# Performance work log

Hardware: AMD Instinct MI355X
Metric: run time of the kernel (lower is better)

The kernel has to match this reference:

```python
import jax, jax.numpy as jnp
import numpy as np

NUM_EXPERTS = 8
HIDDEN = 2048
EXPERT_DIM = 4096
R = 64
LORA_ALPHA = 16
SCALING = LORA_ALPHA / R
TOKENS_PER_EXPERT = 1024


def setup_inputs() -> dict:
    key = jax.random.key(0)
    ks = jax.random.split(key, 7)
    s = lambda shape: 1.0 / np.sqrt(shape[-1])
    return {
        "hidden_states": jax.random.normal(ks[0], (NUM_EXPERTS * TOKENS_PER_EXPERT, HIDDEN), jnp.float32),
        "W_gu": jax.random.normal(ks[1], (2 * EXPERT_DIM, HIDDEN), jnp.float32) * s((HIDDEN,)),
        "A_gu": jax.random.normal(ks[2], (R, HIDDEN), jnp.float32) * s((HIDDEN,)),
        "B_gu": jax.random.normal(ks[3], (2 * EXPERT_DIM, R), jnp.float32) * 0.01,
        "W_d": jax.random.normal(ks[4], (HIDDEN, EXPERT_DIM), jnp.float32) * s((EXPERT_DIM,)),
        "A_d": jax.random.normal(ks[5], (R, EXPERT_DIM), jnp.float32) * s((EXPERT_DIM,)),
        "B_d": jax.random.normal(ks[6], (HIDDEN, R), jnp.float32) * 0.01,
    }


def _lora_linear(x, W, A, B):
    # y = x @ W^T + scaling * (x @ A^T) @ B^T   (nn.Linear convention, no dropout)
    return x @ W.T + (x @ A.T) @ B.T * SCALING


def reference(hidden_states, W_gu, A_gu, B_gu, W_d, A_d, B_d):
    # (E, N, H)
    x = hidden_states.reshape(NUM_EXPERTS, -1, HIDDEN)
    gate_up = _lora_linear(x, W_gu, A_gu, B_gu)          # (E, N, 2*D)
    gate, up = jnp.split(gate_up, 2, axis=-1)             # each (E, N, D)
    h = up * jax.nn.silu(gate)                            # SwiGLU
    out = _lora_linear(h, W_d, A_d, B_d)                  # (E, N, H)
    return out.reshape(-1, HIDDEN)
```

## Files before the change

### kernel.cpp

```cpp
#include <hip/hip_runtime.h>
#include <stdint.h>

typedef __bf16 bf16_t;
typedef __bf16 bf16x8 __attribute__((ext_vector_type(8)));
typedef __bf16 bf16x4 __attribute__((ext_vector_type(4)));
typedef float f32x4 __attribute__((ext_vector_type(4)));

#define GLOAD16(gp, lp)                                                        \
    __builtin_amdgcn_global_load_lds(                                          \
        (const __attribute__((address_space(1))) void*)(gp),                   \
        (__attribute__((address_space(3))) void*)(lp), 16, 0, 0)


__global__ __launch_bounds__(256) void cvt_all_kernel(
    const float* __restrict__ x, const float* __restrict__ Wgu,
    const float* __restrict__ Bgu, const float* __restrict__ Wd,
    const float* __restrict__ Bd, const float* __restrict__ Agu,
    const float* __restrict__ Ad, bf16_t* __restrict__ X1,
    bf16_t* __restrict__ W1, bf16_t* __restrict__ W2,
    bf16_t* __restrict__ Abf, bf16_t* __restrict__ Adbf) {
    int b = blockIdx.x;
    const float* src;
    bf16_t* dst;
    int cshift, cmask, ldd, coff, lb;
    if (b < 16384) {
        src = x; dst = X1; cshift = 11; cmask = 2047; ldd = 2112; coff = 0; lb = b;
    } else if (b < 32768) {
        src = Wgu; dst = W1; cshift = 11; cmask = 2047; ldd = 2112; coff = 0; lb = b - 16384;
    } else if (b < 33280) {
        src = Bgu; dst = W1; cshift = 6; cmask = 63; ldd = 2112; coff = 2048; lb = b - 32768;
    } else if (b < 41472) {
        src = Wd; dst = W2; cshift = 12; cmask = 4095; ldd = 4160; coff = 0; lb = b - 33280;
    } else if (b < 41600) {
        src = Bd; dst = W2; cshift = 6; cmask = 63; ldd = 4160; coff = 4096; lb = b - 41472;
    } else if (b < 41728) {
        src = Agu; dst = Abf; cshift = 11; cmask = 2047; ldd = 2048; coff = 0; lb = b - 41600;
    } else {
        src = Ad; dst = Adbf; cshift = 12; cmask = 4095; ldd = 4096; coff = 0; lb = b - 41728;
    }
    int idx = (lb * 256 + threadIdx.x) << 2;
    int r = idx >> cshift;
    int c = idx & cmask;
    float4 v = *(const float4*)(src + idx);
    bf16x4 o = {(bf16_t)v.x, (bf16_t)v.y, (bf16_t)v.z, (bf16_t)v.w};
    *(bf16x4*)(dst + (size_t)r * ldd + coff + c) = o;
}

__global__ __launch_bounds__(256) void lora_kernel(const bf16_t* __restrict__ A,
                                                   int lda,
                                                   const bf16_t* __restrict__ Bw,
                                                   int K, bf16_t* __restrict__ dst,
                                                   int ldd, int coff) {
    __shared__ __align__(16) bf16_t As[64 * 64];
    __shared__ __align__(16) bf16_t Bs[64 * 64];
    const int t = threadIdx.x;
    const int m0 = blockIdx.x * 64;
    const int lane = t & 63, w = t >> 6;
    const int ln15 = lane & 15, q = lane >> 4;

    const int lrow = t >> 3;
    const int lchunk = (t & 7) ^ (lrow & 7);
    const bf16_t* gaL = A + (size_t)(m0 + lrow) * lda + lchunk * 8;
    const bf16_t* gbL = Bw + (size_t)lrow * K + lchunk * 8;
    bf16_t* lA = As + t * 8;
    bf16_t* lB = Bs + t * 8;

    const f32x4 z = {0.f, 0.f, 0.f, 0.f};
    f32x4 acc[4];
#pragma unroll
    for (int j = 0; j < 4; ++j) acc[j] = z;

    int aoffs[2], boffs[2][4];
#pragma unroll
    for (int s = 0; s < 2; ++s) {
        int rowa = w * 16 + ln15;
        aoffs[s] = rowa * 64 + (((q + 4 * s) ^ (rowa & 7)) << 3);
#pragma unroll
        for (int j = 0; j < 4; ++j) {
            int rowb = j * 16 + ln15;
            boffs[s][j] = rowb * 64 + (((q + 4 * s) ^ (rowb & 7)) << 3);
        }
    }

    for (int kt = 0; kt < K; kt += 64) {
        GLOAD16(gaL, lA);
        GLOAD16(gaL + (size_t)32 * lda, lA + 32 * 64);
        GLOAD16(gbL, lB);
        GLOAD16(gbL + (size_t)32 * K, lB + 32 * 64);
        __syncthreads();
#pragma unroll
        for (int s = 0; s < 2; ++s) {
            bf16x8 av = *(const bf16x8*)(As + aoffs[s]);
#pragma unroll
            for (int j = 0; j < 4; ++j) {
                bf16x8 bv = *(const bf16x8*)(Bs + boffs[s][j]);
                acc[j] = __builtin_amdgcn_mfma_f32_16x16x32_bf16(av, bv, acc[j], 0, 0, 0);
            }
        }
        __syncthreads();
        gaL += 64;
        gbL += 64;
    }

#pragma unroll
    for (int j = 0; j < 4; ++j)
#pragma unroll
        for (int rg = 0; rg < 4; ++rg) {
            int m = m0 + w * 16 + q * 4 + rg;
            dst[(size_t)m * ldd + coff + j * 16 + ln15] = (bf16_t)(acc[j][rg] * 0.25f);
        }
}

__global__ __launch_bounds__(256, 4) void gemm1_kernel(const bf16_t* __restrict__ X,
                                                       const bf16_t* __restrict__ Wc,
                                                       bf16_t* __restrict__ X2) {
    constexpr int LDA = 2112, LDW = 2112, LDX2 = 4160, K = 2112;
    __shared__ __align__(16) bf16_t As[128 * 64];
    __shared__ __align__(16) bf16_t Bs[128 * 64];
    const int t = threadIdx.x;
    const int n0 = blockIdx.x * 64;
    const int m0 = blockIdx.y * 128;
    const int lane = t & 63, w = t >> 6, wr = w >> 1, wc = w & 1;
    const int ln15 = lane & 15, q = lane >> 4;

    const int lrow = t >> 3;
    const int lchunk = (t & 7) ^ (lrow & 7);
    const bf16_t* gaL = X + (size_t)(m0 + lrow) * LDA + lchunk * 8;
    const bf16_t* gbgL = Wc + (size_t)(n0 + lrow) * LDW + lchunk * 8;
    const bf16_t* gbuL = Wc + (size_t)(4096 + n0 + lrow) * LDW + lchunk * 8;
    bf16_t* lA = As + t * 8;
    bf16_t* lB = Bs + t * 8;

    const f32x4 z = {0.f, 0.f, 0.f, 0.f};
    f32x4 accg[4][2], accu[4][2];
#pragma unroll
    for (int i = 0; i < 4; ++i)
#pragma unroll
        for (int j = 0; j < 2; ++j) {
            accg[i][j] = z;
            accu[i][j] = z;
        }

    int aoffs[2][4], bgoffs[2][2];
#pragma unroll
    for (int s = 0; s < 2; ++s) {
#pragma unroll
        for (int i = 0; i < 4; ++i) {
            int row = wr * 64 + i * 16 + ln15;
            aoffs[s][i] = row * 64 + (((q + 4 * s) ^ (row & 7)) << 3);
        }
#pragma unroll
        for (int j = 0; j < 2; ++j) {
            int row = wc * 32 + j * 16 + ln15;
            bgoffs[s][j] = row * 64 + (((q + 4 * s) ^ (row & 7)) << 3);
        }
    }

    for (int kt = 0; kt < K; kt += 64) {
        GLOAD16(gaL, lA);
        GLOAD16(gaL + (size_t)32 * LDA, lA + 32 * 64);
        GLOAD16(gaL + (size_t)64 * LDA, lA + 64 * 64);
        GLOAD16(gaL + (size_t)96 * LDA, lA + 96 * 64);
        GLOAD16(gbgL, lB);
        GLOAD16(gbgL + (size_t)32 * LDW, lB + 32 * 64);
        GLOAD16(gbuL, lB + 64 * 64);
        GLOAD16(gbuL + (size_t)32 * LDW, lB + 96 * 64);
        __syncthreads();
#pragma unroll
        for (int s = 0; s < 2; ++s) {
            bf16x8 av[4], bg[2], bu[2];
#pragma unroll
            for (int i = 0; i < 4; ++i) av[i] = *(const bf16x8*)(As + aoffs[s][i]);
#pragma unroll
            for (int j = 0; j < 2; ++j) {
                bg[j] = *(const bf16x8*)(Bs + bgoffs[s][j]);
                bu[j] = *(const bf16x8*)(Bs + bgoffs[s][j] + 64 * 64);
            }
#pragma unroll
            for (int i = 0; i < 4; ++i)
#pragma unroll
                for (int j = 0; j < 2; ++j) {
                    accg[i][j] = __builtin_amdgcn_mfma_f32_16x16x32_bf16(av[i], bg[j], accg[i][j], 0, 0, 0);
                    accu[i][j] = __builtin_amdgcn_mfma_f32_16x16x32_bf16(av[i], bu[j], accu[i][j], 0, 0, 0);
                }
        }
        __syncthreads();
        gaL += 64;
        gbgL += 64;
        gbuL += 64;
    }

#pragma unroll
    for (int i = 0; i < 4; ++i)
#pragma unroll
        for (int j = 0; j < 2; ++j)
#pragma unroll
            for (int rg = 0; rg < 4; ++rg) {
                int m = m0 + wr * 64 + i * 16 + q * 4 + rg;
                int d = n0 + wc * 32 + j * 16 + ln15;
                float g = accg[i][j][rg];
                float u = accu[i][j][rg];
                float h = u * g / (1.f + __expf(-g));
                X2[(size_t)m * LDX2 + d] = (bf16_t)h;
            }
}

__global__ __launch_bounds__(256, 4) void gemm2_kernel(const bf16_t* __restrict__ X2,
                                                       const bf16_t* __restrict__ Wdc,
                                                       float* __restrict__ out) {
    constexpr int LDA = 4160, LDB = 4160, K = 4160, LDO = 2048;
    __shared__ __align__(16) bf16_t As[128 * 64];
    __shared__ __align__(16) bf16_t Bs[128 * 64];
    const int t = threadIdx.x;
    const int n0 = blockIdx.x * 128;
    const int m0 = blockIdx.y * 128;
    const int lane = t & 63, w = t >> 6, wr = w >> 1, wc = w & 1;
    const int ln15 = lane & 15, q = lane >> 4;

    const int lrow = t >> 3;
    const int lchunk = (t & 7) ^ (lrow & 7);
    const bf16_t* gaL = X2 + (size_t)(m0 + lrow) * LDA + lchunk * 8;
    const bf16_t* gbL = Wdc + (size_t)(n0 + lrow) * LDB + lchunk * 8;
    bf16_t* lA = As + t * 8;
    bf16_t* lB = Bs + t * 8;

    const f32x4 z = {0.f, 0.f, 0.f, 0.f};
    f32x4 acc[4][4];
#pragma unroll
    for (int i = 0; i < 4; ++i)
#pragma unroll
        for (int j = 0; j < 4; ++j) acc[i][j] = z;

    int aoffs[2][4], boffs[2][4];
#pragma unroll
    for (int s = 0; s < 2; ++s)
#pragma unroll
        for (int i = 0; i < 4; ++i) {
            int rowa = wr * 64 + i * 16 + ln15;
            int rowb = wc * 64 + i * 16 + ln15;
            aoffs[s][i] = rowa * 64 + (((q + 4 * s) ^ (rowa & 7)) << 3);
            boffs[s][i] = rowb * 64 + (((q + 4 * s) ^ (rowb & 7)) << 3);
        }

    for (int kt = 0; kt < K; kt += 64) {
        GLOAD16(gaL, lA);
        GLOAD16(gaL + (size_t)32 * LDA, lA + 32 * 64);
        GLOAD16(gaL + (size_t)64 * LDA, lA + 64 * 64);
        GLOAD16(gaL + (size_t)96 * LDA, lA + 96 * 64);
        GLOAD16(gbL, lB);
        GLOAD16(gbL + (size_t)32 * LDB, lB + 32 * 64);
        GLOAD16(gbL + (size_t)64 * LDB, lB + 64 * 64);
        GLOAD16(gbL + (size_t)96 * LDB, lB + 96 * 64);
        __syncthreads();
#pragma unroll
        for (int s = 0; s < 2; ++s) {
            bf16x8 av[4], bv[4];
#pragma unroll
            for (int i = 0; i < 4; ++i) {
                av[i] = *(const bf16x8*)(As + aoffs[s][i]);
                bv[i] = *(const bf16x8*)(Bs + boffs[s][i]);
            }
#pragma unroll
            for (int i = 0; i < 4; ++i)
#pragma unroll
                for (int j = 0; j < 4; ++j)
                    acc[i][j] = __builtin_amdgcn_mfma_f32_16x16x32_bf16(av[i], bv[j], acc[i][j], 0, 0, 0);
        }
        __syncthreads();
        gaL += 64;
        gbL += 64;
    }

#pragma unroll
    for (int i = 0; i < 4; ++i)
#pragma unroll
        for (int j = 0; j < 4; ++j)
#pragma unroll
            for (int rg = 0; rg < 4; ++rg) {
                int m = m0 + wr * 64 + i * 16 + q * 4 + rg;
                int n = n0 + wc * 64 + j * 16 + ln15;
                out[(size_t)m * LDO + n] = acc[i][j][rg];
            }
}

extern "C" void kernel_launch(void* const* d_in, const int* in_sizes, int n_in,
                              void* d_out, int out_size, void* d_ws, size_t ws_size,
                              hipStream_t stream) {
    const float* x = (const float*)d_in[0];
    const float* Wgu = (const float*)d_in[1];
    const float* Agu = (const float*)d_in[2];
    const float* Bgu = (const float*)d_in[3];
    const float* Wd = (const float*)d_in[4];
    const float* Ad = (const float*)d_in[5];
    const float* Bd = (const float*)d_in[6];
    float* out = (float*)d_out;

    char* ws = (char*)d_ws;
    bf16_t* X1 = (bf16_t*)(ws);
    bf16_t* W1 = (bf16_t*)(ws + 34603008);
    bf16_t* X2 = (bf16_t*)(ws + 69206016);
    bf16_t* W2 = (bf16_t*)(ws + 137363456);
    bf16_t* Abf = (bf16_t*)(ws + 154402816);
    bf16_t* Adbf = (bf16_t*)(ws + 154664960);

    cvt_all_kernel<<<41984, 256, 0, stream>>>(x, Wgu, Bgu, Wd, Bd, Agu, Ad,
                                              X1, W1, W2, Abf, Adbf);

    lora_kernel<<<128, 256, 0, stream>>>(X1, 2112, Abf, 2048, X1, 2112, 2048);
    gemm1_kernel<<<dim3(64, 64), 256, 0, stream>>>(X1, W1, X2);
    lora_kernel<<<128, 256, 0, stream>>>(X2, 4160, Adbf, 4096, X2, 4160, 4096);
    gemm2_kernel<<<dim3(16, 64), 256, 0, stream>>>(X2, W2, out);
}
```

Baseline: 635.3 us.

## Double-buffer LDS with half-depth K tiles in LoRA and both GEMM kernels

Measured after the change: 720.8 us. 1.13x slower.

```diff
diff --git a/kernel.cpp b/kernel.cpp
--- a/kernel.cpp
+++ b/kernel.cpp
@@ -51,55 +51,57 @@
                                                    const bf16_t* __restrict__ Bw,
                                                    int K, bf16_t* __restrict__ dst,
                                                    int ldd, int coff) {
-    __shared__ __align__(16) bf16_t As[64 * 64];
-    __shared__ __align__(16) bf16_t Bs[64 * 64];
+    __shared__ __align__(16) bf16_t As0[64 * 32];
+    __shared__ __align__(16) bf16_t Bs0[64 * 32];
+    __shared__ __align__(16) bf16_t As1[64 * 32];
+    __shared__ __align__(16) bf16_t Bs1[64 * 32];
     const int t = threadIdx.x;
     const int m0 = blockIdx.x * 64;
     const int lane = t & 63, w = t >> 6;
     const int ln15 = lane & 15, q = lane >> 4;
 
-    const int lrow = t >> 3;
-    const int lchunk = (t & 7) ^ (lrow & 7);
-    const bf16_t* gaL = A + (size_t)(m0 + lrow) * lda + lchunk * 8;
-    const bf16_t* gbL = Bw + (size_t)lrow * K + lchunk * 8;
-    bf16_t* lA = As + t * 8;
-    bf16_t* lB = Bs + t * 8;
+    const int lrow = t >> 2;
+    const int lchunk = (t & 3) ^ ((t >> 3) & 3);
+    const bf16_t* ga = A + (size_t)(m0 + lrow) * lda + lchunk * 8;
+    const bf16_t* gb = Bw + (size_t)lrow * K + lchunk * 8;
+    const int ld = t * 8;
 
     const f32x4 z = {0.f, 0.f, 0.f, 0.f};
     f32x4 acc[4];
 #pragma unroll
     for (int j = 0; j < 4; ++j) acc[j] = z;
 
-    int aoffs[2], boffs[2][4];
-#pragma unroll
-    for (int s = 0; s < 2; ++s) {
-        int rowa = w * 16 + ln15;
-        aoffs[s] = rowa * 64 + (((q + 4 * s) ^ (rowa & 7)) << 3);
-#pragma unroll
-        for (int j = 0; j < 4; ++j) {
-            int rowb = j * 16 + ln15;
-            boffs[s][j] = rowb * 64 + (((q + 4 * s) ^ (rowb & 7)) << 3);
-        }
-    }
-
+    const int arow = w * 16 + ln15;
+    const int aoff = arow * 32 + ((q ^ ((arow >> 1) & 3)) << 3);
+    int boff[4];
+#pragma unroll
+    for (int j = 0; j < 4; ++j) {
+        int r = j * 16 + ln15;
+        boff[j] = r * 32 + ((q ^ ((r >> 1) & 3)) << 3);
+    }
+
+#define LORA_COMPUTE(AS, BS)                                                   \
+    {                                                                          \
+        bf16x8 av = *(const bf16x8*)(AS + aoff);                               \
+        _Pragma("unroll") for (int j = 0; j < 4; ++j) {                        \
+            bf16x8 bv = *(const bf16x8*)(BS + boff[j]);                        \
+            acc[j] = __builtin_amdgcn_mfma_f32_16x16x32_bf16(av, bv, acc[j], 0, 0, 0); \
+        }                                                                      \
+    }
+
+    GLOAD16(ga, As0 + ld);
+    GLOAD16(gb, Bs0 + ld);
     for (int kt = 0; kt < K; kt += 64) {
-        GLOAD16(gaL, lA);
-        GLOAD16(gaL + (size_t)32 * lda, lA + 32 * 64);
-        GLOAD16(gbL, lB);
-        GLOAD16(gbL + (size_t)32 * K, lB + 32 * 64);
-        __syncthreads();
-#pragma unroll
-        for (int s = 0; s < 2; ++s) {
-            bf16x8 av = *(const bf16x8*)(As + aoffs[s]);
-#pragma unroll
-            for (int j = 0; j < 4; ++j) {
-                bf16x8 bv = *(const bf16x8*)(Bs + boffs[s][j]);
-                acc[j] = __builtin_amdgcn_mfma_f32_16x16x32_bf16(av, bv, acc[j], 0, 0, 0);
-            }
-        }
-        __syncthreads();
-        gaL += 64;
-        gbL += 64;
+        __syncthreads();
+        GLOAD16(ga + kt + 32, As1 + ld);
+        GLOAD16(gb + kt + 32, Bs1 + ld);
+        LORA_COMPUTE(As0, Bs0)
+        __syncthreads();
+        if (kt + 64 < K) {
+            GLOAD16(ga + kt + 64, As0 + ld);
+            GLOAD16(gb + kt + 64, Bs0 + ld);
+        }
+        LORA_COMPUTE(As1, Bs1)
     }
 
 #pragma unroll
@@ -115,21 +117,23 @@
                                                        const bf16_t* __restrict__ Wc,
                                                        bf16_t* __restrict__ X2) {
     constexpr int LDA = 2112, LDW = 2112, LDX2 = 4160, K = 2112;
-    __shared__ __align__(16) bf16_t As[128 * 64];
-    __shared__ __align__(16) bf16_t Bs[128 * 64];
+    __shared__ __align__(16) bf16_t As0[128 * 32];
+    __shared__ __align__(16) bf16_t Bs0[128 * 32];
+    __shared__ __align__(16) bf16_t As1[128 * 32];
+    __shared__ __align__(16) bf16_t Bs1[128 * 32];
     const int t = threadIdx.x;
     const int n0 = blockIdx.x * 64;
     const int m0 = blockIdx.y * 128;
     const int lane = t & 63, w = t >> 6, wr = w >> 1, wc = w & 1;
     const int ln15 = lane & 15, q = lane >> 4;
 
-    const int lrow = t >> 3;
-    const int lchunk = (t & 7) ^ (lrow & 7);
-    const bf16_t* gaL = X + (size_t)(m0 + lrow) * LDA + lchunk * 8;
-    const bf16_t* gbgL = Wc + (size_t)(n0 + lrow) * LDW + lchunk * 8;
-    const bf16_t* gbuL = Wc + (size_t)(4096 + n0 + lrow) * LDW + lchunk * 8;
-    bf16_t* lA = As + t * 8;
-    bf16_t* lB = Bs + t * 8;
+    const int lrow = t >> 2;
+    const int lchunk = (t & 3) ^ ((t >> 3) & 3);
+    const bf16_t* ga = X + (size_t)(m0 + lrow) * LDA + lchunk * 8;
+    const bf16_t* ga2 = ga + (size_t)64 * LDA;
+    const bf16_t* gbg = Wc + (size_t)(n0 + lrow) * LDW + lchunk * 8;
+    const bf16_t* gbu = Wc + (size_t)(4096 + n0 + lrow) * LDW + lchunk * 8;
+    const int ld = t * 8;
 
     const f32x4 z = {0.f, 0.f, 0.f, 0.f};
     f32x4 accg[4][2], accu[4][2];
@@ -141,53 +145,53 @@
             accu[i][j] = z;
         }
 
-    int aoffs[2][4], bgoffs[2][2];
-#pragma unroll
-    for (int s = 0; s < 2; ++s) {
-#pragma unroll
-        for (int i = 0; i < 4; ++i) {
-            int row = wr * 64 + i * 16 + ln15;
-            aoffs[s][i] = row * 64 + (((q + 4 * s) ^ (row & 7)) << 3);
-        }
-#pragma unroll
-        for (int j = 0; j < 2; ++j) {
-            int row = wc * 32 + j * 16 + ln15;
-            bgoffs[s][j] = row * 64 + (((q + 4 * s) ^ (row & 7)) << 3);
-        }
-    }
-
+    int aoff[4], bgoff[2];
+#pragma unroll
+    for (int i = 0; i < 4; ++i) {
+        int row = wr * 64 + i * 16 + ln15;
+        aoff[i] = row * 32 + ((q ^ ((row >> 1) & 3)) << 3);
+    }
+#pragma unroll
+    for (int j = 0; j < 2; ++j) {
+        int row = wc * 32 + j * 16 + ln15;
+        bgoff[j] = row * 32 + ((q ^ ((row >> 1) & 3)) << 3);
+    }
+
+#define G1_COMPUTE(AS, BS)                                                     \
+    {                                                                          \
+        bf16x8 av[4], bg[2], bu[2];                                            \
+        _Pragma("unroll") for (int i = 0; i < 4; ++i)                          \
+            av[i] = *(const bf16x8*)(AS + aoff[i]);                            \
+        _Pragma("unroll") for (int j = 0; j < 2; ++j) {                        \
+            bg[j] = *(const bf16x8*)(BS + bgoff[j]);                           \
+            bu[j] = *(const bf16x8*)(BS + bgoff[j] + 2048);                    \
+        }                                                                      \
+        _Pragma("unroll") for (int i = 0; i < 4; ++i)                          \
+            _Pragma("unroll") for (int j = 0; j < 2; ++j) {                    \
+                accg[i][j] = __builtin_amdgcn_mfma_f32_16x16x32_bf16(av[i], bg[j], accg[i][j], 0, 0, 0); \
+                accu[i][j] = __builtin_amdgcn_mfma_f32_16x16x32_bf16(av[i], bu[j], accu[i][j], 0, 0, 0); \
+            }                                                                  \
+    }
+
+    GLOAD16(ga, As0 + ld);
+    GLOAD16(ga2, As0 + 2048 + ld);
+    GLOAD16(gbg, Bs0 + ld);
+    GLOAD16(gbu, Bs0 + 2048 + ld);
     for (int kt = 0; kt < K; kt += 64) {
-        GLOAD16(gaL, lA);
-        GLOAD16(gaL + (size_t)32 * LDA, lA + 32 * 64);
-        GLOAD16(gaL + (size_t)64 * LDA, lA + 64 * 64);
-        GLOAD16(gaL + (size_t)96 * LDA, lA + 96 * 64);
-        GLOAD16(gbgL, lB);
-        GLOAD16(gbgL + (size_t)32 * LDW, lB + 32 * 64);
-        GLOAD16(gbuL, lB + 64 * 64);
-        GLOAD16(gbuL + (size_t)32 * LDW, lB + 96 * 64);
-        __syncthreads();
-#pragma unroll
-        for (int s = 0; s < 2; ++s) {
-            bf16x8 av[4], bg[2], bu[2];
-#pragma unroll
-            for (int i = 0; i < 4; ++i) av[i] = *(const bf16x8*)(As + aoffs[s][i]);
-#pragma unroll
-            for (int j = 0; j < 2; ++j) {
-                bg[j] = *(const bf16x8*)(Bs + bgoffs[s][j]);
-                bu[j] = *(const bf16x8*)(Bs + bgoffs[s][j] + 64 * 64);
-            }
-#pragma unroll
-            for (int i = 0; i < 4; ++i)
-#pragma unroll
-                for (int j = 0; j < 2; ++j) {
-                    accg[i][j] = __builtin_amdgcn_mfma_f32_16x16x32_bf16(av[i], bg[j], accg[i][j], 0, 0, 0);
-                    accu[i][j] = __builtin_amdgcn_mfma_f32_16x16x32_bf16(av[i], bu[j], accu[i][j], 0, 0, 0);
-                }
-        }
-        __syncthreads();
-        gaL += 64;
-        gbgL += 64;
-        gbuL += 64;
+        __syncthreads();
+        GLOAD16(ga + kt + 32, As1 + ld);
+        GLOAD16(ga2 + kt + 32, As1 + 2048 + ld);
+        GLOAD16(gbg + kt + 32, Bs1 + ld);
+        GLOAD16(gbu + kt + 32, Bs1 + 2048 + ld);
+        G1_COMPUTE(As0, Bs0)
+        __syncthreads();
+        if (kt + 64 < K) {
+            GLOAD16(ga + kt + 64, As0 + ld);
+            GLOAD16(ga2 + kt + 64, As0 + 2048 + ld);
+            GLOAD16(gbg + kt + 64, Bs0 + ld);
+            GLOAD16(gbu + kt + 64, Bs0 + 2048 + ld);
+        }
+        G1_COMPUTE(As1, Bs1)
     }
 
 #pragma unroll
@@ -209,20 +213,23 @@
                                                        const bf16_t* __restrict__ Wdc,
                                                        float* __restrict__ out) {
     constexpr int LDA = 4160, LDB = 4160, K = 4160, LDO = 2048;
-    __shared__ __align__(16) bf16_t As[128 * 64];
-    __shared__ __align__(16) bf16_t Bs[128 * 64];
+    __shared__ __align__(16) bf16_t As0[128 * 32];
+    __shared__ __align__(16) bf16_t Bs0[128 * 32];
+    __shared__ __align__(16) bf16_t As1[128 * 32];
+    __shared__ __align__(16) bf16_t Bs1[128 * 32];
     const int t = threadIdx.x;
     const int n0 = blockIdx.x * 128;
     const int m0 = blockIdx.y * 128;
     const int lane = t & 63, w = t >> 6, wr = w >> 1, wc = w & 1;
     const int ln15 = lane & 15, q = lane >> 4;
 
-    const int lrow = t >> 3;
-    const int lchunk = (t & 7) ^ (lrow & 7);
-    const bf16_t* gaL = X2 + (size_t)(m0 + lrow) * LDA + lchunk * 8;
-    const bf16_t* gbL = Wdc + (size_t)(n0 + lrow) * LDB + lchunk * 8;
-    bf16_t* lA = As + t * 8;
-    bf16_t* lB = Bs + t * 8;
+    const int lrow = t >> 2;
+    const int lchunk = (t & 3) ^ ((t >> 3) & 3);
+    const bf16_t* ga = X2 + (size_t)(m0 + lrow) * LDA + lchunk * 8;
+    const bf16_t* ga2 = ga + (size_t)64 * LDA;
+    const bf16_t* gb = Wdc + (size_t)(n0 + lrow) * LDB + lchunk * 8;
+    const bf16_t* gb2 = gb + (size_t)64 * LDB;
+    const int ld = t * 8;
 
     const f32x4 z = {0.f, 0.f, 0.f, 0.f};
     f32x4 acc[4][4];
@@ -231,44 +238,46 @@
 #pragma unroll
         for (int j = 0; j < 4; ++j) acc[i][j] = z;
 
-    int aoffs[2][4], boffs[2][4];
-#pragma unroll
-    for (int s = 0; s < 2; ++s)
-#pragma unroll
-        for (int i = 0; i < 4; ++i) {
-            int rowa = wr * 64 + i * 16 + ln15;
-            int rowb = wc * 64 + i * 16 + ln15;
-            aoffs[s][i] = rowa * 64 + (((q + 4 * s) ^ (rowa & 7)) << 3);
-            boffs[s][i] = rowb * 64 + (((q + 4 * s) ^ (rowb & 7)) << 3);
-        }
-
+    int aoff[4], boff[4];
+#pragma unroll
+    for (int i = 0; i < 4; ++i) {
+        int rowa = wr * 64 + i * 16 + ln15;
+        int rowb = wc * 64 + i * 16 + ln15;
+        aoff[i] = rowa * 32 + ((q ^ ((rowa >> 1) & 3)) << 3);
+        boff[i] = rowb * 32 + ((q ^ ((rowb >> 1) & 3)) << 3);
+    }
+
+#define G2_COMPUTE(AS, BS)                                                     \
+    {                                                                          \
+        bf16x8 av[4], bv[4];                                                   \
+        _Pragma("unroll") for (int i = 0; i < 4; ++i) {                        \
+            av[i] = *(const bf16x8*)(AS + aoff[i]);                            \
+            bv[i] = *(const bf16x8*)(BS + boff[i]);                            \
+        }                                                                      \
+        _Pragma("unroll") for (int i = 0; i < 4; ++i)                          \
+            _Pragma("unroll") for (int j = 0; j < 4; ++j)                      \
+                acc[i][j] = __builtin_amdgcn_mfma_f32_16x16x32_bf16(av[i], bv[j], acc[i][j], 0, 0, 0); \
+    }
+
+    GLOAD16(ga, As0 + ld);
+    GLOAD16(ga2, As0 + 2048 + ld);
+    GLOAD16(gb, Bs0 + ld);
+    GLOAD16(gb2, Bs0 + 2048 + ld);
     for (int kt = 0; kt < K; kt += 64) {
-        GLOAD16(gaL, lA);
-        GLOAD16(gaL + (size_t)32 * LDA, lA + 32 * 64);
-        GLOAD16(gaL + (size_t)64 * LDA, lA + 64 * 64);
-        GLOAD16(gaL + (size_t)96 * LDA, lA + 96 * 64);
-        GLOAD16(gbL, lB);
-        GLOAD16(gbL + (size_t)32 * LDB, lB + 32 * 64);
-        GLOAD16(gbL + (size_t)64 * LDB, lB + 64 * 64);
-        GLOAD16(gbL + (size_t)96 * LDB, lB + 96 * 64);
-        __syncthreads();
-#pragma unroll
-        for (int s = 0; s < 2; ++s) {
-            bf16x8 av[4], bv[4];
-#pragma unroll
-            for (int i = 0; i < 4; ++i) {
-                av[i] = *(const bf16x8*)(As + aoffs[s][i]);
-                bv[i] = *(const bf16x8*)(Bs + boffs[s][i]);
-            }
-#pragma unroll
-            for (int i = 0; i < 4; ++i)
-#pragma unroll
-                for (int j = 0; j < 4; ++j)
-                    acc[i][j] = __builtin_amdgcn_mfma_f32_16x16x32_bf16(av[i], bv[j], acc[i][j], 0, 0, 0);
-        }
-        __syncthreads();
-        gaL += 64;
-        gbL += 64;
+        __syncthreads();
+        GLOAD16(ga + kt + 32, As1 + ld);
+        GLOAD16(ga2 + kt + 32, As1 + 2048 + ld);
+        GLOAD16(gb + kt + 32, Bs1 + ld);
+        GLOAD16(gb2 + kt + 32, Bs1 + 2048 + ld);
+        G2_COMPUTE(As0, Bs0)
+        __syncthreads();
+        if (kt + 64 < K) {
+            GLOAD16(ga + kt + 64, As0 + ld);
+            GLOAD16(ga2 + kt + 64, As0 + 2048 + ld);
+            GLOAD16(gb + kt + 64, Bs0 + ld);
+            GLOAD16(gb2 + kt + 64, Bs0 + 2048 + ld);
+        }
+        G2_COMPUTE(As1, Bs1)
     }
 
 #pragma unroll
```
